# Optimization experiments

Measured on AMD Instinct MI355X. Metric: run time of the kernel, lower is better.

Reference implementation:

```python
import jax, jax.numpy as jnp
import numpy as np

TSZ, BSZ, E, H = 1024, 8, 1024, 16


def setup_inputs() -> dict:
    key = jax.random.key(0)
    ks = jax.random.split(key, 7)
    s = 0.02
    return {
        "q": jax.random.normal(ks[0], (TSZ, BSZ, E), jnp.float32),
        "k": jax.random.normal(ks[1], (TSZ, BSZ, E), jnp.float32),
        "v": jax.random.normal(ks[2], (TSZ, BSZ, E), jnp.float32),
        "in_proj_weight": jax.random.normal(ks[3], (3 * E, E), jnp.float32) * s,
        "in_proj_bias": jax.random.normal(ks[4], (3 * E,), jnp.float32) * s,
        "out_proj_weight": jax.random.normal(ks[5], (E, E), jnp.float32) * s,
        "out_proj_bias": jax.random.normal(ks[6], (E,), jnp.float32) * s,
        "num_heads": H,
    }


def reference(q, k, v, in_proj_weight, in_proj_bias, out_proj_weight, out_proj_bias, num_heads):
    tsz, bsz, embed_dim = q.shape
    head_dim = embed_dim // num_heads
    scaling = float(head_dim) ** -0.5

    # in-projections (F.linear: x @ W.T + b), weight sliced into q/k/v chunks
    qp = q @ in_proj_weight[:embed_dim].T + in_proj_bias[:embed_dim]
    kp = k @ in_proj_weight[embed_dim:2 * embed_dim].T + in_proj_bias[embed_dim:2 * embed_dim]
    vp = v @ in_proj_weight[2 * embed_dim:].T + in_proj_bias[2 * embed_dim:]
    qp = qp * scaling

    # (tsz, bsz, E) -> (bsz*H, tsz, head_dim)
    def to_heads(x):
        return x.reshape(tsz, bsz * num_heads, head_dim).transpose(1, 0, 2)

    qh, kh, vh = to_heads(qp), to_heads(kp), to_heads(vp)

    # scaled dot-product attention (no mask, dropout p=0)
    scores = jnp.einsum('bqd,bkd->bqk', qh, kh)  # [bsz*H, tsz, tsz]
    weights = jax.nn.softmax(scores, axis=-1)
    attn = jnp.einsum('bqk,bkd->bqd', weights, vh)

    # back to (tsz, bsz, E), then out projection
    attn = attn.transpose(1, 0, 2).reshape(tsz, bsz, embed_dim)
    out = attn @ out_proj_weight.T + out_proj_bias
    return out
```

## Files before the change

### kernel.cpp

```cpp
#include <hip/hip_runtime.h>

typedef __bf16 bf16;
typedef __attribute__((ext_vector_type(8))) __bf16 v8bf;
typedef __attribute__((ext_vector_type(4))) __bf16 v4bf;
typedef __attribute__((ext_vector_type(4))) float f32x4;

static_assert(sizeof(v8bf) == 16, "v8bf must be 16B");

#define MFMA16(a, b, c) __builtin_amdgcn_mfma_f32_16x16x32_bf16((a), (b), (c), 0, 0, 0)

__device__ __forceinline__ void async_lds16(const bf16* g, bf16* l) {
  __builtin_amdgcn_global_load_lds(
      (__attribute__((address_space(1))) void*)(g),
      (__attribute__((address_space(3))) void*)(l), 16, 0, 0);
}

__global__ __launch_bounds__(256) void cvt_kernel(
    const float* __restrict__ q, const float* __restrict__ k,
    const float* __restrict__ v, const float* __restrict__ wi,
    const float* __restrict__ wo, bf16* __restrict__ xq, bf16* __restrict__ xk,
    bf16* __restrict__ xv, bf16* __restrict__ Wb, bf16* __restrict__ Wob) {
  int idx = blockIdx.x * 256 + threadIdx.x;
  const float4* src;
  v4bf* dst;
  int off;
  if (idx < 2097152)      { src = (const float4*)q;  dst = (v4bf*)xq;  off = idx; }
  else if (idx < 4194304) { src = (const float4*)k;  dst = (v4bf*)xk;  off = idx - 2097152; }
  else if (idx < 6291456) { src = (const float4*)v;  dst = (v4bf*)xv;  off = idx - 4194304; }
  else if (idx < 7077888) { src = (const float4*)wi; dst = (v4bf*)Wb;  off = idx - 6291456; }
  else                    { src = (const float4*)wo; dst = (v4bf*)Wob; off = idx - 7077888; }
  float4 f = src[off];
  v4bf b;
  b[0] = (bf16)f.x; b[1] = (bf16)f.y; b[2] = (bf16)f.z; b[3] = (bf16)f.w;
  dst[off] = b;
}

__global__ __launch_bounds__(256) void qkv_proj_kernel(
    const bf16* __restrict__ xq, const bf16* __restrict__ xk,
    const bf16* __restrict__ xv, const bf16* __restrict__ Wb,
    const float* __restrict__ bias, bf16* __restrict__ oq,
    bf16* __restrict__ ok, bf16* __restrict__ ov) {
  __shared__ bf16 Asm[128 * 32];
  __shared__ bf16 Bsm[128 * 32];
  const int c = blockIdx.z;
  const bf16* X = (c == 0) ? xq : (c == 1) ? xk : xv;
  bf16* outp = (c == 0) ? oq : (c == 1) ? ok : ov;
  const int n0 = blockIdx.x * 128;
  const int m0 = blockIdx.y * 128;
  const int tid = threadIdx.x;
  const int w = tid >> 6, l = tid & 63, quad = l >> 4, lr = l & 15;
  const int wm = (w & 1) * 64, wn = (w >> 1) * 64;
  const bf16* Wbase = Wb + ((size_t)(c * 1024 + n0)) * 1024;

  f32x4 acc[4][4] = {};
  for (int kt = 0; kt < 32; ++kt) {
    const int k0 = kt * 32;
#pragma unroll
    for (int i = 0; i < 2; ++i) {
      const int chunk = w * 128 + i * 64 + l;
      const int row = chunk >> 2, kp = chunk & 3;
      async_lds16(X + (size_t)(m0 + row) * 1024 + k0 + kp * 8,
                  &Asm[(w * 128 + i * 64) * 8]);
      async_lds16(Wbase + (size_t)row * 1024 + k0 + kp * 8,
                  &Bsm[(w * 128 + i * 64) * 8]);
    }
    __syncthreads();
    v8bf af[4], bfm[4];
#pragma unroll
    for (int rt = 0; rt < 4; ++rt)
      af[rt] = *(const v8bf*)&Asm[(wm + rt * 16 + lr) * 32 + quad * 8];
#pragma unroll
    for (int ct = 0; ct < 4; ++ct)
      bfm[ct] = *(const v8bf*)&Bsm[(wn + ct * 16 + lr) * 32 + quad * 8];
#pragma unroll
    for (int rt = 0; rt < 4; ++rt)
#pragma unroll
      for (int ct = 0; ct < 4; ++ct)
        acc[rt][ct] = MFMA16(af[rt], bfm[ct], acc[rt][ct]);
    __syncthreads();
  }

  const float scale = (c == 0) ? 0.125f : 1.0f;
#pragma unroll
  for (int rt = 0; rt < 4; ++rt) {
#pragma unroll
    for (int ct = 0; ct < 4; ++ct) {
      const int n = n0 + wn + ct * 16 + lr;
      const float bn = bias[c * 1024 + n];
      const int h = n >> 6, d = n & 63;
#pragma unroll
      for (int j = 0; j < 4; ++j) {
        const int m = m0 + wm + rt * 16 + quad * 4 + j;
        const int t = m >> 3, b = m & 7;
        const float val = (acc[rt][ct][j] + bn) * scale;
        outp[((size_t)((b * 16 + h) * 1024 + t)) * 64 + d] = (bf16)val;
      }
    }
  }
}

__global__ __launch_bounds__(256) void transpose_v_kernel(const bf16* __restrict__ vin,
                                                          bf16* __restrict__ vout) {
  __shared__ bf16 tile[64][72];
  const int bh = blockIdx.x;
  const int t0 = blockIdx.y * 64;
  const int tid = threadIdx.x;
  const int row = tid >> 2, cg = (tid & 3) * 16;
  const bf16* src = vin + ((size_t)bh * 1024 + t0 + row) * 64 + cg;
#pragma unroll
  for (int i = 0; i < 2; ++i) {
    v8bf x = *(const v8bf*)(src + i * 8);
#pragma unroll
    for (int jj = 0; jj < 8; ++jj) tile[row][cg + i * 8 + jj] = x[jj];
  }
  __syncthreads();
  const int d = tid >> 2, tg = (tid & 3) * 16;
  bf16* dst = vout + ((size_t)bh * 64 + d) * 1024 + t0 + tg;
  v8bf o0, o1;
#pragma unroll
  for (int i = 0; i < 8; ++i) o0[i] = tile[tg + i][d];
#pragma unroll
  for (int i = 0; i < 8; ++i) o1[i] = tile[tg + 8 + i][d];
  *(v8bf*)dst = o0;
  *(v8bf*)(dst + 8) = o1;
}

#define KSTR 72
#define VSTR 136

__global__ __launch_bounds__(256, 3) void attn_kernel(const bf16* __restrict__ qh,
                                                      const bf16* __restrict__ kh,
                                                      const bf16* __restrict__ vT,
                                                      bf16* __restrict__ attn_out) {
  __shared__ bf16 Ksm[128 * KSTR];
  __shared__ bf16 Vsm[64 * VSTR];
  __shared__ bf16 Psm[4 * 16 * VSTR];
  const int bh = blockIdx.y;
  const int t0 = blockIdx.x * 64;
  const int tid = threadIdx.x;
  const int w = tid >> 6, l = tid & 63, quad = l >> 4, lr = l & 15;
  const int qrow0 = t0 + w * 16;

  const bf16* khead = kh + (size_t)bh * 1024 * 64;
  const bf16* vhead = vT + (size_t)bh * 64 * 1024;

  const size_t qbase = ((size_t)bh * 1024 + qrow0 + lr) * 64 + quad * 8;
  const v8bf bq0 = *(const v8bf*)(qh + qbase);
  const v8bf bq1 = *(const v8bf*)(qh + qbase + 32);

  const int krow = tid >> 1, kd = (tid & 1) * 32;
  const int vrow = tid >> 2, vk = (tid & 3) * 32;
  const bf16* kg = khead + (size_t)krow * 64 + kd;
  const bf16* vg = vhead + (size_t)vrow * 1024 + vk;
  bf16* Kw = &Ksm[krow * KSTR + kd];
  bf16* Vw = &Vsm[vrow * VSTR + vk];
  bf16* Pw = &Psm[w * 16 * VSTR];

  v8bf kst[4], vst[4];
#pragma unroll
  for (int i = 0; i < 4; ++i) kst[i] = *(const v8bf*)(kg + i * 8);
#pragma unroll
  for (int i = 0; i < 4; ++i) vst[i] = *(const v8bf*)(vg + i * 8);

  float m_run = -3.0e38f, l_run = 0.0f;
  f32x4 oacc[4] = {};

  for (int c = 0; c < 8; ++c) {
    __syncthreads();
#pragma unroll
    for (int i = 0; i < 4; ++i) *(v8bf*)(Kw + i * 8) = kst[i];
#pragma unroll
    for (int i = 0; i < 4; ++i) *(v8bf*)(Vw + i * 8) = vst[i];
    __syncthreads();
    if (c < 7) {
      const bf16* kg2 = kg + (size_t)(c + 1) * 128 * 64;
      const bf16* vg2 = vg + (c + 1) * 128;
#pragma unroll
      for (int i = 0; i < 4; ++i) kst[i] = *(const v8bf*)(kg2 + i * 8);
#pragma unroll
      for (int i = 0; i < 4; ++i) vst[i] = *(const v8bf*)(vg2 + i * 8);
    }

    f32x4 s[8];
#pragma unroll
    for (int kt = 0; kt < 8; ++kt) {
      const v8bf ak0 = *(const v8bf*)&Ksm[(kt * 16 + lr) * KSTR + quad * 8];
      const v8bf ak1 = *(const v8bf*)&Ksm[(kt * 16 + lr) * KSTR + 32 + quad * 8];
      f32x4 a = {};
      a = MFMA16(ak0, bq0, a);
      a = MFMA16(ak1, bq1, a);
      s[kt] = a;
    }

    float mc = -3.0e38f;
#pragma unroll
    for (int kt = 0; kt < 8; ++kt)
#pragma unroll
      for (int j = 0; j < 4; ++j) mc = fmaxf(mc, s[kt][j]);
    mc = fmaxf(mc, __shfl_xor(mc, 16));
    mc = fmaxf(mc, __shfl_xor(mc, 32));
    const float m_new = fmaxf(m_run, mc);
    const float alpha = __expf(m_run - m_new);
    m_run = m_new;

    float sc = 0.0f;
#pragma unroll
    for (int kt = 0; kt < 8; ++kt) {
      v4bf pb;
#pragma unroll
      for (int j = 0; j < 4; ++j) {
        const float p = __expf(s[kt][j] - m_new);
        sc += p;
        pb[j] = (bf16)p;
      }
      *(v4bf*)(Pw + lr * VSTR + kt * 16 + quad * 4) = pb;
    }
    sc += __shfl_xor(sc, 16);
    sc += __shfl_xor(sc, 32);
    l_run = l_run * alpha + sc;

#pragma unroll
    for (int j = 0; j < 4; ++j) {
      const float aj = __shfl(alpha, quad * 4 + j);
#pragma unroll
      for (int dt = 0; dt < 4; ++dt) oacc[dt][j] *= aj;
    }

#pragma unroll
    for (int ks = 0; ks < 4; ++ks) {
      const v8bf pa = *(const v8bf*)(Pw + lr * VSTR + ks * 32 + quad * 8);
#pragma unroll
      for (int dt = 0; dt < 4; ++dt) {
        const v8bf vb = *(const v8bf*)&Vsm[(dt * 16 + lr) * VSTR + ks * 32 + quad * 8];
        oacc[dt] = MFMA16(pa, vb, oacc[dt]);
      }
    }
  }

  const float inv = 1.0f / l_run;
  const int b = bh >> 4, h = bh & 15;
#pragma unroll
  for (int j = 0; j < 4; ++j) {
    const float ij = __shfl(inv, quad * 4 + j);
    const int t = qrow0 + quad * 4 + j;
#pragma unroll
    for (int dt = 0; dt < 4; ++dt)
      attn_out[((size_t)(t * 8 + b)) * 1024 + h * 64 + dt * 16 + lr] =
          (bf16)(oacc[dt][j] * ij);
  }
}

__global__ __launch_bounds__(256) void out_proj_kernel(const bf16* __restrict__ A,
                                                       const bf16* __restrict__ Wob,
                                                       const float* __restrict__ bias,
                                                       float* __restrict__ out) {
  __shared__ bf16 Asm[128 * 32];
  __shared__ bf16 Bsm[128 * 32];
  const int n0 = blockIdx.x * 128;
  const int m0 = blockIdx.y * 128;
  const int tid = threadIdx.x;
  const int w = tid >> 6, l = tid & 63, quad = l >> 4, lr = l & 15;
  const int wm = (w & 1) * 64, wn = (w >> 1) * 64;

  f32x4 acc[4][4] = {};
  for (int kt = 0; kt < 32; ++kt) {
    const int k0 = kt * 32;
#pragma unroll
    for (int i = 0; i < 2; ++i) {
      const int chunk = w * 128 + i * 64 + l;
      const int row = chunk >> 2, kp = chunk & 3;
      async_lds16(A + (size_t)(m0 + row) * 1024 + k0 + kp * 8,
                  &Asm[(w * 128 + i * 64) * 8]);
      async_lds16(Wob + (size_t)(n0 + row) * 1024 + k0 + kp * 8,
                  &Bsm[(w * 128 + i * 64) * 8]);
    }
    __syncthreads();
    v8bf af[4], bfm[4];
#pragma unroll
    for (int rt = 0; rt < 4; ++rt)
      af[rt] = *(const v8bf*)&Asm[(wm + rt * 16 + lr) * 32 + quad * 8];
#pragma unroll
    for (int ct = 0; ct < 4; ++ct)
      bfm[ct] = *(const v8bf*)&Bsm[(wn + ct * 16 + lr) * 32 + quad * 8];
#pragma unroll
    for (int rt = 0; rt < 4; ++rt)
#pragma unroll
      for (int ct = 0; ct < 4; ++ct)
        acc[rt][ct] = MFMA16(af[rt], bfm[ct], acc[rt][ct]);
    __syncthreads();
  }

#pragma unroll
  for (int rt = 0; rt < 4; ++rt)
#pragma unroll
    for (int ct = 0; ct < 4; ++ct) {
      const int n = n0 + wn + ct * 16 + lr;
      const float bn = bias[n];
#pragma unroll
      for (int j = 0; j < 4; ++j) {
        const int m = m0 + wm + rt * 16 + quad * 4 + j;
        out[(size_t)m * 1024 + n] = acc[rt][ct][j] + bn;
      }
    }
}

extern "C" void kernel_launch(void* const* d_in, const int* in_sizes, int n_in,
                              void* d_out, int out_size, void* d_ws, size_t ws_size,
                              hipStream_t stream) {
  const float* q  = (const float*)d_in[0];
  const float* k  = (const float*)d_in[1];
  const float* v  = (const float*)d_in[2];
  const float* wi = (const float*)d_in[3];
  const float* bi = (const float*)d_in[4];
  const float* wo = (const float*)d_in[5];
  const float* bo = (const float*)d_in[6];
  float* out = (float*)d_out;
  char* ws = (char*)d_ws;
  const size_t MB = (size_t)1 << 20;
  bf16* Wb     = (bf16*)(ws + 0 * MB);
  bf16* Wob    = (bf16*)(ws + 6 * MB);
  bf16* wsq    = (bf16*)(ws + 8 * MB);
  bf16* wsk    = (bf16*)(ws + 24 * MB);
  bf16* wsv    = (bf16*)(ws + 40 * MB);
  bf16* xv     = (bf16*)(ws + 56 * MB);
  bf16* wsvT   = (bf16*)(ws + 56 * MB);
  bf16* xq     = (bf16*)d_out;
  bf16* xk     = (bf16*)((char*)d_out + 16 * MB);
  bf16* wsattn = wsv;

  cvt_kernel<<<dim3(28672), dim3(256), 0, stream>>>(q, k, v, wi, wo, xq, xk, xv, Wb, Wob);
  qkv_proj_kernel<<<dim3(8, 64, 3), dim3(256), 0, stream>>>(xq, xk, xv, Wb, bi, wsq, wsk, wsv);
  transpose_v_kernel<<<dim3(128, 16), dim3(256), 0, stream>>>(wsv, wsvT);
  attn_kernel<<<dim3(16, 128), dim3(256), 0, stream>>>(wsq, wsk, wsvT, wsattn);
  out_proj_kernel<<<dim3(8, 64), dim3(256), 0, stream>>>(wsattn, Wob, bo, out);
}
```

Before: 345.5 us.

## Swizzle GEMM LDS layout and remap block indices for XCD-aware L2 locality

```diff
diff --git a/kernel.cpp b/kernel.cpp
--- a/kernel.cpp
+++ b/kernel.cpp
@@ -42,36 +42,45 @@
     bf16* __restrict__ ok, bf16* __restrict__ ov) {
   __shared__ bf16 Asm[128 * 32];
   __shared__ bf16 Bsm[128 * 32];
-  const int c = blockIdx.z;
+  const int L = blockIdx.x;
+  const int rX = L & 7, rest = L >> 3;
+  const int m0 = (rX * 8 + (rest & 7)) * 128;
+  const int n0 = ((rest >> 3) & 7) * 128;
+  const int c = rest >> 6;
   const bf16* X = (c == 0) ? xq : (c == 1) ? xk : xv;
   bf16* outp = (c == 0) ? oq : (c == 1) ? ok : ov;
-  const int n0 = blockIdx.x * 128;
-  const int m0 = blockIdx.y * 128;
   const int tid = threadIdx.x;
   const int w = tid >> 6, l = tid & 63, quad = l >> 4, lr = l & 15;
   const int wm = (w & 1) * 64, wn = (w >> 1) * 64;
+  const int sw = quad ^ ((lr >> 1) & 3);
   const bf16* Wbase = Wb + ((size_t)(c * 1024 + n0)) * 1024;
+
+  int srow[2], sk[2];
+#pragma unroll
+  for (int i = 0; i < 2; ++i) {
+    const int chunk = w * 128 + i * 64 + l;
+    srow[i] = chunk >> 2;
+    sk[i] = ((chunk & 3) ^ ((srow[i] >> 1) & 3)) * 8;
+  }
 
   f32x4 acc[4][4] = {};
   for (int kt = 0; kt < 32; ++kt) {
     const int k0 = kt * 32;
 #pragma unroll
     for (int i = 0; i < 2; ++i) {
-      const int chunk = w * 128 + i * 64 + l;
-      const int row = chunk >> 2, kp = chunk & 3;
-      async_lds16(X + (size_t)(m0 + row) * 1024 + k0 + kp * 8,
+      async_lds16(X + (size_t)(m0 + srow[i]) * 1024 + k0 + sk[i],
                   &Asm[(w * 128 + i * 64) * 8]);
-      async_lds16(Wbase + (size_t)row * 1024 + k0 + kp * 8,
+      async_lds16(Wbase + (size_t)srow[i] * 1024 + k0 + sk[i],
                   &Bsm[(w * 128 + i * 64) * 8]);
     }
     __syncthreads();
     v8bf af[4], bfm[4];
 #pragma unroll
     for (int rt = 0; rt < 4; ++rt)
-      af[rt] = *(const v8bf*)&Asm[(wm + rt * 16 + lr) * 32 + quad * 8];
+      af[rt] = *(const v8bf*)&Asm[(wm + rt * 16 + lr) * 32 + sw * 8];
 #pragma unroll
     for (int ct = 0; ct < 4; ++ct)
-      bfm[ct] = *(const v8bf*)&Bsm[(wn + ct * 16 + lr) * 32 + quad * 8];
+      bfm[ct] = *(const v8bf*)&Bsm[(wn + ct * 16 + lr) * 32 + sw * 8];
 #pragma unroll
     for (int rt = 0; rt < 4; ++rt)
 #pragma unroll
@@ -135,8 +144,9 @@
   __shared__ bf16 Ksm[128 * KSTR];
   __shared__ bf16 Vsm[64 * VSTR];
   __shared__ bf16 Psm[4 * 16 * VSTR];
-  const int bh = blockIdx.y;
-  const int t0 = blockIdx.x * 64;
+  const int L = blockIdx.x;
+  const int bh = (L & 7) * 16 + ((L >> 3) & 15);
+  const int t0 = (L >> 7) * 64;
   const int tid = threadIdx.x;
   const int w = tid >> 6, l = tid & 63, quad = l >> 4, lr = l & 15;
   const int qrow0 = t0 + w * 16;
@@ -256,32 +266,40 @@
                                                        float* __restrict__ out) {
   __shared__ bf16 Asm[128 * 32];
   __shared__ bf16 Bsm[128 * 32];
-  const int n0 = blockIdx.x * 128;
-  const int m0 = blockIdx.y * 128;
+  const int L = blockIdx.x;
+  const int m0 = ((L & 7) * 8 + ((L >> 3) & 7)) * 128;
+  const int n0 = (L >> 6) * 128;
   const int tid = threadIdx.x;
   const int w = tid >> 6, l = tid & 63, quad = l >> 4, lr = l & 15;
   const int wm = (w & 1) * 64, wn = (w >> 1) * 64;
+  const int sw = quad ^ ((lr >> 1) & 3);
+
+  int srow[2], sk[2];
+#pragma unroll
+  for (int i = 0; i < 2; ++i) {
+    const int chunk = w * 128 + i * 64 + l;
+    srow[i] = chunk >> 2;
+    sk[i] = ((chunk & 3) ^ ((srow[i] >> 1) & 3)) * 8;
+  }
 
   f32x4 acc[4][4] = {};
   for (int kt = 0; kt < 32; ++kt) {
     const int k0 = kt * 32;
 #pragma unroll
     for (int i = 0; i < 2; ++i) {
-      const int chunk = w * 128 + i * 64 + l;
-      const int row = chunk >> 2, kp = chunk & 3;
-      async_lds16(A + (size_t)(m0 + row) * 1024 + k0 + kp * 8,
+      async_lds16(A + (size_t)(m0 + srow[i]) * 1024 + k0 + sk[i],
                   &Asm[(w * 128 + i * 64) * 8]);
-      async_lds16(Wob + (size_t)(n0 + row) * 1024 + k0 + kp * 8,
+      async_lds16(Wob + (size_t)(n0 + srow[i]) * 1024 + k0 + sk[i],
                   &Bsm[(w * 128 + i * 64) * 8]);
     }
     __syncthreads();
     v8bf af[4], bfm[4];
 #pragma unroll
     for (int rt = 0; rt < 4; ++rt)
-      af[rt] = *(const v8bf*)&Asm[(wm + rt * 16 + lr) * 32 + quad * 8];
+      af[rt] = *(const v8bf*)&Asm[(wm + rt * 16 + lr) * 32 + sw * 8];
 #pragma unroll
     for (int ct = 0; ct < 4; ++ct)
-      bfm[ct] = *(const v8bf*)&Bsm[(wn + ct * 16 + lr) * 32 + quad * 8];
+      bfm[ct] = *(const v8bf*)&Bsm[(wn + ct * 16 + lr) * 32 + sw * 8];
 #pragma unroll
     for (int rt = 0; rt < 4; ++rt)
 #pragma unroll
@@ -329,8 +347,8 @@
   bf16* wsattn = wsv;
 
   cvt_kernel<<<dim3(28672), dim3(256), 0, stream>>>(q, k, v, wi, wo, xq, xk, xv, Wb, Wob);
-  qkv_proj_kernel<<<dim3(8, 64, 3), dim3(256), 0, stream>>>(xq, xk, xv, Wb, bi, wsq, wsk, wsv);
+  qkv_proj_kernel<<<dim3(1536), dim3(256), 0, stream>>>(xq, xk, xv, Wb, bi, wsq, wsk, wsv);
   transpose_v_kernel<<<dim3(128, 16), dim3(256), 0, stream>>>(wsv, wsvT);
-  attn_kernel<<<dim3(16, 128), dim3(256), 0, stream>>>(wsq, wsk, wsvT, wsattn);
-  out_proj_kernel<<<dim3(8, 64), dim3(256), 0, stream>>>(wsattn, Wob, bo, out);
-}
+  attn_kernel<<<dim3(2048), dim3(256), 0, stream>>>(wsq, wsk, wsvT, wsattn);
+  out_proj_kernel<<<dim3(512), dim3(256), 0, stream>>>(wsattn, Wob, bo, out);
+}
```

Result: faster. 321.2 us (-7.0%).
